# Performance work log

Hardware: AMD Instinct MI355X
Metric: run time of the kernel (lower is better)

The kernel has to match this reference:

```python
import jax, jax.numpy as jnp
import numpy as np

N_HEADS = 16
N_KV_HEADS = 4
HEAD_DIM = 128
ROPE_BASE = 10000.0


def _rms_norm(x):
    eps = jnp.asarray(jnp.finfo(x.dtype).eps, x.dtype)
    return x * jax.lax.rsqrt(jnp.mean(x * x, axis=-1, keepdims=True) + eps)


def _rope_tables(T, dtype):
    d = HEAD_DIM
    inv_freq = 1.0 / (ROPE_BASE ** (jnp.arange(0, d, 2, dtype=jnp.float32) / d))
    freqs = jnp.outer(jnp.arange(T, dtype=jnp.float32), inv_freq)  # [T, d/2]
    return jnp.cos(freqs).astype(dtype), jnp.sin(freqs).astype(dtype)


def _apply_rope(x, cos, sin):
    # x: [B, H, T, D]; cos/sin: [T, D/2]
    d = x.shape[-1] // 2
    x1, x2 = x[..., :d], x[..., d:]
    return jnp.concatenate((x1 * cos + x2 * sin, -x1 * sin + x2 * cos), axis=-1)


def setup_inputs() -> dict:
    key = jax.random.key(0)
    ks = jax.random.split(key, 5)
    B, T, C = 2, 2048, 2048
    kv_dim = N_KV_HEADS * HEAD_DIM
    s = 0.02
    return {
        "x": jax.random.normal(ks[0], (B, T, C), jnp.float32),
        "Wq": jax.random.normal(ks[1], (C, C), jnp.float32) * s,
        "Wk": jax.random.normal(ks[2], (kv_dim, C), jnp.float32) * s,
        "Wv": jax.random.normal(ks[3], (kv_dim, C), jnp.float32) * s,
        "Wo": jax.random.normal(ks[4], (C, C), jnp.float32) * s,
    }


def reference(x, Wq, Wk, Wv, Wo):
    B, T, C = x.shape
    g = N_HEADS // N_KV_HEADS

    # QKV projections (torch Linear: x @ W.T), split into heads -> [B, H, T, D]
    q = (x @ Wq.T).reshape(B, T, N_HEADS, HEAD_DIM).transpose(0, 2, 1, 3)
    k = (x @ Wk.T).reshape(B, T, N_KV_HEADS, HEAD_DIM).transpose(0, 2, 1, 3)
    v = (x @ Wv.T).reshape(B, T, N_KV_HEADS, HEAD_DIM).transpose(0, 2, 1, 3)

    # QK RMSNorm (no learned weight)
    q, k = _rms_norm(q), _rms_norm(k)

    # RoPE
    cos, sin = _rope_tables(T, q.dtype)
    q, k = _apply_rope(q, cos, sin), _apply_rope(k, cos, sin)

    # GQA: expand kv heads
    k = jnp.repeat(k, g, axis=1)
    v = jnp.repeat(v, g, axis=1)

    # causal SDPA
    scale = 1.0 / jnp.sqrt(jnp.asarray(HEAD_DIM, q.dtype))
    scores = jnp.einsum("bhqd,bhkd->bhqk", q, k) * scale
    mask = jnp.tril(jnp.ones((T, T), bool))
    scores = jnp.where(mask, scores, jnp.asarray(-jnp.inf, scores.dtype))
    att = jax.nn.softmax(scores, axis=-1)
    y = jnp.einsum("bhqk,bhkd->bhqd", att, v)

    y = y.transpose(0, 2, 1, 3).reshape(B, T, C)
    return y @ Wo.T
```

## Files before the change

### kernel.cpp

```cpp
#include <hip/hip_runtime.h>
#include <hip/hip_bf16.h>
#include <cstdint>
#include <math.h>

#define DEVINL __device__ __forceinline__

typedef __attribute__((ext_vector_type(8))) __bf16 bf16x8;
typedef __attribute__((ext_vector_type(4))) float floatx4;

constexpr int TB = 2;
constexpr int TT = 2048;
constexpr int TC = 2048;
constexpr int NH = 16, NKV = 4, HD = 128;
constexpr int MR = TB * TT;
constexpr int NQ = NH * HD;
constexpr int NK = NKV * HD;
constexpr int NQKV = NQ + 2 * NK;

DEVINL unsigned bfbits(float f) {
  unsigned u = __builtin_bit_cast(unsigned, f);
  return (u + 0x7FFFu + ((u >> 16) & 1u)) >> 16;
}
DEVINL int pk2(float a, float b) {
  union { __hip_bfloat162 h; int i; } u;
  u.h = __float22bfloat162_rn(float2{a, b});
  return u.i;
}
DEVINL void gl_lds16(const __hip_bfloat16* g, __hip_bfloat16* l) {
  __builtin_amdgcn_global_load_lds(
      (const __attribute__((address_space(1))) unsigned int*)g,
      (__attribute__((address_space(3))) unsigned int*)l, 16, 0, 0);
}
DEVINL floatx4 mfma16(bf16x8 a, bf16x8 b, floatx4 c) {
  return __builtin_amdgcn_mfma_f32_16x16x32_bf16(a, b, c, 0, 0, 0);
}
DEVINL void cstore(float* p, float v) { *p = v; }
DEVINL void cstore(__hip_bfloat16* p, float v) { *(unsigned short*)p = (unsigned short)bfbits(v); }

__global__ __launch_bounds__(256) void k_cvt5(
    const float* __restrict__ s0, const float* __restrict__ s1,
    const float* __restrict__ s2, const float* __restrict__ s3,
    const float* __restrict__ s4,
    __hip_bfloat16* __restrict__ d0, __hip_bfloat16* __restrict__ d1,
    __hip_bfloat16* __restrict__ d2, __hip_bfloat16* __restrict__ d3,
    __hip_bfloat16* __restrict__ d4) {
  const float* s;
  __hip_bfloat16* d;
  int n;
  switch (blockIdx.y) {
    case 0: s = s0; d = d0; n = MR * TC; break;
    case 1: s = s1; d = d1; n = NQ * TC; break;
    case 2: s = s2; d = d2; n = NK * TC; break;
    case 3: s = s3; d = d3; n = NK * TC; break;
    default: s = s4; d = d4; n = TC * TC; break;
  }
  int i = (blockIdx.x * 256 + threadIdx.x) * 4;
  if (i >= n) return;
  float4 v = *(const float4*)(s + i);
  ushort4 o;
  o.x = (unsigned short)bfbits(v.x);
  o.y = (unsigned short)bfbits(v.y);
  o.z = (unsigned short)bfbits(v.z);
  o.w = (unsigned short)bfbits(v.w);
  *(ushort4*)(d + i) = o;
}

template <typename OUT_T>
__global__ __launch_bounds__(256, 2) void k_gemm_bt(
    const __hip_bfloat16* __restrict__ A, const __hip_bfloat16* __restrict__ B,
    OUT_T* __restrict__ C, int M, int N, int K) {
  __shared__ __align__(16) __hip_bfloat16 As[128 * 32];
  __shared__ __align__(16) __hip_bfloat16 Bs[128 * 32];
  const int tid = threadIdx.x;
  const int lane = tid & 63, w = tid >> 6;
  const int q15 = lane & 15, quad = lane >> 4;
  const int wm = w >> 1, wn = w & 1;
  const int tm = blockIdx.y, tn = blockIdx.x;

  const int r0 = tid >> 2, c0 = (tid & 3) * 8;
  const __hip_bfloat16* a0 = A + (size_t)(tm * 128 + r0) * K + c0;
  const __hip_bfloat16* a1 = A + (size_t)(tm * 128 + r0 + 64) * K + c0;
  const __hip_bfloat16* b0 = B + (size_t)(tn * 128 + r0) * K + c0;
  const __hip_bfloat16* b1 = B + (size_t)(tn * 128 + r0 + 64) * K + c0;
  __hip_bfloat16* lA0 = As + (tid & ~63) * 8;
  __hip_bfloat16* lA1 = As + 2048 + (tid & ~63) * 8;
  __hip_bfloat16* lB0 = Bs + (tid & ~63) * 8;
  __hip_bfloat16* lB1 = Bs + 2048 + (tid & ~63) * 8;

  floatx4 acc[4][4] = {};
  for (int k0 = 0; k0 < K; k0 += 32) {
    __syncthreads();
    gl_lds16(a0 + k0, lA0);
    gl_lds16(a1 + k0, lA1);
    gl_lds16(b0 + k0, lB0);
    gl_lds16(b1 + k0, lB1);
    __syncthreads();
    bf16x8 af[4], bfr[4];
#pragma unroll
    for (int i = 0; i < 4; i++)
      af[i] = *(const bf16x8*)(As + (wm * 64 + i * 16 + q15) * 32 + quad * 8);
#pragma unroll
    for (int i = 0; i < 4; i++)
      bfr[i] = *(const bf16x8*)(Bs + (wn * 64 + i * 16 + q15) * 32 + quad * 8);
#pragma unroll
    for (int mi = 0; mi < 4; mi++)
#pragma unroll
      for (int ni = 0; ni < 4; ni++)
        acc[mi][ni] = mfma16(af[mi], bfr[ni], acc[mi][ni]);
  }
#pragma unroll
  for (int mi = 0; mi < 4; mi++) {
    int row0 = tm * 128 + wm * 64 + mi * 16 + quad * 4;
#pragma unroll
    for (int ni = 0; ni < 4; ni++) {
      int col = tn * 128 + wn * 64 + ni * 16 + q15;
#pragma unroll
      for (int r = 0; r < 4; r++)
        cstore(C + (size_t)(row0 + r) * N + col, acc[mi][ni][r]);
    }
  }
}

constexpr int ROPE_BLOCKS = (MR * 20) / 4;
__global__ __launch_bounds__(256) void k_prep(
    const __hip_bfloat16* __restrict__ qkv,
    __hip_bfloat16* __restrict__ q_l, __hip_bfloat16* __restrict__ k_l,
    __hip_bfloat16* __restrict__ vt) {
  if (blockIdx.x < ROPE_BLOCKS) {
    int gw = (blockIdx.x * 256 + threadIdx.x) >> 6;
    int lane = threadIdx.x & 63;
    int head = gw % 20;
    int bt = gw / 20;
    int b = bt >> 11, t = bt & (TT - 1);
    bool isq = head < NH;
    int h = isq ? head : head - NH;
    const __hip_bfloat16* src = qkv + (size_t)bt * NQKV + (isq ? h * HD : NQ + h * HD);
    float x1 = __bfloat162float(src[lane]);
    float x2 = __bfloat162float(src[lane + 64]);
    float ss = x1 * x1 + x2 * x2;
#pragma unroll
    for (int m = 1; m < 64; m <<= 1) ss += __shfl_xor(ss, m, 64);
    float rinv = rsqrtf(ss * (1.0f / 128.0f) + 1.1920928955078125e-07f);
    float ang = (float)t * exp2f((float)lane * -(13.287712379549449f / 64.0f));
    float sv = sinf(ang), cv = cosf(ang);
    float scale = isq ? (1.4426950408889634f * 0.08838834764831845f) : 1.0f;
    float o1 = (x1 * cv + x2 * sv) * rinv * scale;
    float o2 = (x2 * cv - x1 * sv) * rinv * scale;
    __hip_bfloat16* dst = isq ? q_l + ((size_t)(b * NH + h) * TT + t) * HD
                              : k_l + ((size_t)(b * NKV + h) * TT + t) * HD;
    *(unsigned short*)(dst + lane) = (unsigned short)bfbits(o1);
    *(unsigned short*)(dst + lane + 64) = (unsigned short)bfbits(o2);
  } else {
    __shared__ __hip_bfloat16 tile[64][130];
    int bid = blockIdx.x - ROPE_BLOCKS;
    int t0 = (bid & 31) * 64;
    int hk = (bid >> 5) & 3;
    int b = bid >> 7;
    int tid = threadIdx.x;
#pragma unroll
    for (int j = 0; j < 32; j++) {
      int e = j * 256 + tid;
      int tt = e >> 7, d = e & 127;
      tile[tt][d] = qkv[(size_t)(b * TT + t0 + tt) * NQKV + NQ + NK + hk * HD + d];
    }
    __syncthreads();
#pragma unroll
    for (int j = 0; j < 32; j++) {
      int e = j * 256 + tid;
      int d = e >> 6, tt = e & 63;
      vt[(((size_t)(b * NKV + hk)) * HD + d) * TT + t0 + tt] = tile[tt][d];
    }
  }
}

__global__ __launch_bounds__(256, 2) void k_attn(
    const __hip_bfloat16* __restrict__ q_l, const __hip_bfloat16* __restrict__ k_l,
    const __hip_bfloat16* __restrict__ vt_l, __hip_bfloat16* __restrict__ y) {
  __shared__ __align__(16) __hip_bfloat16 Ks[2][64 * 128];
  __shared__ __align__(16) __hip_bfloat16 Vs[2][128 * 64];
  __shared__ __align__(16) __hip_bfloat16 Ps[4][32 * 64];
  const int tid = threadIdx.x, lane = tid & 63, w = tid >> 6;
  const int q15 = lane & 15, quad = lane >> 4;
  const int id = blockIdx.x;
  const int qt = (TT / 128 - 1) - (id >> 5);
  const int h = id & 15, b = (id >> 4) & 1;
  const int hk = h >> 2;
  const int nkb = 2 * qt + 2;

  const __hip_bfloat16* kbase = k_l + (size_t)(b * NKV + hk) * TT * HD;
  const __hip_bfloat16* vbase = vt_l + (size_t)(b * NKV + hk) * HD * TT;
  const __hip_bfloat16* qbase = q_l + ((size_t)(b * NH + h) * TT + qt * 128) * HD;

  auto stage = [&](int kb, int buf) {
#pragma unroll
    for (int i = 0; i < 4; i++) {
      int s = i * 256 + tid;
      int rk = s >> 4, ck = s & 15;
      gl_lds16(kbase + (size_t)(kb * 64 + rk) * HD + (ck ^ (rk & 15)) * 8,
               Ks[buf] + (i * 256 + (tid & ~63)) * 8);
      int rv = s >> 3, cv = s & 7;
      gl_lds16(vbase + (size_t)rv * TT + kb * 64 + (cv ^ (rv & 7)) * 8,
               Vs[buf] + (i * 256 + (tid & ~63)) * 8);
    }
  };

  bf16x8 qf[4][2];
#pragma unroll
  for (int dc = 0; dc < 4; dc++)
#pragma unroll
    for (int qh = 0; qh < 2; qh++)
      qf[dc][qh] = *(const bf16x8*)(qbase + (size_t)(w * 32 + qh * 16 + q15) * HD +
                                    dc * 32 + quad * 8);

  __hip_bfloat16* pw = Ps[w];
  const int qrow0 = q15, qrow1 = 16 + q15;
  const int pw_c = 2 * 0 + (quad >> 1);
  const int pw_h = (quad & 1) * 4;

  floatx4 ot[8][2] = {};
  float lsum[2] = {0.0f, 0.0f};
  int cur = 0;
  const int kb_last_w = 2 * qt + (w >> 1);

  for (int kb = 0; kb < nkb; kb++) {
    __syncthreads();
    if (kb == 0) {
      stage(0, cur);
      __syncthreads();
    }
    if (kb + 1 < nkb) stage(kb + 1, cur ^ 1);

    if (kb <= kb_last_w) {
      floatx4 st[4][2] = {};
#pragma unroll
      for (int kt = 0; kt < 4; kt++) {
        int r = kt * 16 + q15;
#pragma unroll
        for (int dc = 0; dc < 4; dc++) {
          int c = dc * 4 + quad;
          bf16x8 kf = *(const bf16x8*)(Ks[cur] + (r * 16 + (c ^ (r & 15))) * 8);
          st[kt][0] = mfma16(kf, qf[dc][0], st[kt][0]);
          st[kt][1] = mfma16(kf, qf[dc][1], st[kt][1]);
        }
      }
      if (kb >= 2 * qt) {
#pragma unroll
        for (int qh = 0; qh < 2; qh++) {
          int qg = qt * 128 + w * 32 + qh * 16 + q15;
#pragma unroll
          for (int kt = 0; kt < 4; kt++)
#pragma unroll
            for (int r = 0; r < 4; r++)
              if (kb * 64 + kt * 16 + quad * 4 + r > qg) st[kt][qh][r] = -INFINITY;
        }
      }
#pragma unroll
      for (int kt = 0; kt < 4; kt++) {
#pragma unroll
        for (int qh = 0; qh < 2; qh++) {
          float p0 = exp2f(st[kt][qh][0]);
          float p1 = exp2f(st[kt][qh][1]);
          float p2 = exp2f(st[kt][qh][2]);
          float p3 = exp2f(st[kt][qh][3]);
          lsum[qh] += (p0 + p1) + (p2 + p3);
          int2 pv;
          pv.x = pk2(p0, p1);
          pv.y = pk2(p2, p3);
          int row = qh * 16 + q15;
          int c4 = (kt * 2 + (quad >> 1)) ^ (row & 7);
          *(int2*)(pw + row * 64 + c4 * 8 + pw_h) = pv;
        }
      }
#pragma unroll
      for (int kc = 0; kc < 2; kc++) {
        bf16x8 pf[2];
#pragma unroll
        for (int qh = 0; qh < 2; qh++) {
          int row = qh * 16 + q15;
          int c4 = (kc * 4 + quad) ^ (row & 7);
          pf[qh] = *(const bf16x8*)(pw + row * 64 + c4 * 8);
        }
#pragma unroll
        for (int dt = 0; dt < 8; dt++) {
          int r = dt * 16 + q15, c = kc * 4 + quad;
          bf16x8 vf = *(const bf16x8*)(Vs[cur] + (r * 8 + (c ^ (r & 7))) * 8);
          ot[dt][0] = mfma16(vf, pf[0], ot[dt][0]);
          ot[dt][1] = mfma16(vf, pf[1], ot[dt][1]);
        }
      }
    }
    cur ^= 1;
  }
#pragma unroll
  for (int qh = 0; qh < 2; qh++) {
    float ls = lsum[qh];
    ls += __shfl_xor(ls, 16, 64);
    ls += __shfl_xor(ls, 32, 64);
    float linv = 1.0f / ls;
    int t = qt * 128 + w * 32 + qh * 16 + q15;
    __hip_bfloat16* yrow = y + (size_t)(b * TT + t) * TC + h * HD;
#pragma unroll
    for (int dt = 0; dt < 8; dt++) {
      int d = dt * 16 + quad * 4;
      ushort4 o;
      o.x = (unsigned short)bfbits(ot[dt][qh][0] * linv);
      o.y = (unsigned short)bfbits(ot[dt][qh][1] * linv);
      o.z = (unsigned short)bfbits(ot[dt][qh][2] * linv);
      o.w = (unsigned short)bfbits(ot[dt][qh][3] * linv);
      *(ushort4*)(yrow + d) = o;
    }
  }
}

extern "C" void kernel_launch(void* const* d_in, const int* in_sizes, int n_in,
                              void* d_out, int out_size, void* d_ws, size_t ws_size,
                              hipStream_t stream) {
  (void)in_sizes; (void)n_in; (void)out_size; (void)ws_size;
  const float* x  = (const float*)d_in[0];
  const float* Wq = (const float*)d_in[1];
  const float* Wk = (const float*)d_in[2];
  const float* Wv = (const float*)d_in[3];
  const float* Wo = (const float*)d_in[4];
  float* out = (float*)d_out;

  char* ws = (char*)d_ws;
  size_t off = 0;
  auto alloc = [&](size_t bytes) {
    void* p = ws + off;
    off += (bytes + 255) & ~(size_t)255;
    return p;
  };
  __hip_bfloat16* xb   = (__hip_bfloat16*)alloc((size_t)MR * TC * 2);
  __hip_bfloat16* wqkv = (__hip_bfloat16*)alloc((size_t)NQKV * TC * 2);
  __hip_bfloat16* wo   = (__hip_bfloat16*)alloc((size_t)TC * TC * 2);
  __hip_bfloat16* qkv  = (__hip_bfloat16*)alloc((size_t)MR * NQKV * 2);
  __hip_bfloat16* q_l  = (__hip_bfloat16*)alloc((size_t)TB * NH * TT * HD * 2);
  __hip_bfloat16* k_l  = (__hip_bfloat16*)alloc((size_t)TB * NKV * TT * HD * 2);
  __hip_bfloat16* vt_l = (__hip_bfloat16*)alloc((size_t)TB * NKV * HD * TT * 2);
  __hip_bfloat16* yb   = (__hip_bfloat16*)alloc((size_t)MR * TC * 2);

  k_cvt5<<<dim3((MR * TC / 4 + 255) / 256, 5), 256, 0, stream>>>(
      x, Wq, Wk, Wv, Wo,
      xb, wqkv, wqkv + (size_t)NQ * TC, wqkv + (size_t)(NQ + NK) * TC, wo);

  k_gemm_bt<__hip_bfloat16><<<dim3(NQKV / 128, MR / 128), 256, 0, stream>>>(
      xb, wqkv, qkv, MR, NQKV, TC);

  k_prep<<<ROPE_BLOCKS + TB * NKV * (TT / 64), 256, 0, stream>>>(qkv, q_l, k_l, vt_l);

  k_attn<<<(TT / 128) * NH * TB, 256, 0, stream>>>(q_l, k_l, vt_l, yb);

  k_gemm_bt<float><<<dim3(TC / 128, MR / 128), 256, 0, stream>>>(
      yb, wo, out, MR, TC, TC);
}
```

Before: 319.3 us.

## Fuse QK RMSNorm, RoPE and V transpose into QKV GEMM epilogue

Replaces the QKV GEMM plus separate prep kernel with a dedicated GEMM whose warps each own 32 rows by a full 128-column head. This lets the epilogue compute the RMS norm, RoPE and scale in registers and write Q/K in head layout and V transposed directly. It removes the intermediate qkv buffer round trip and one kernel launch, at the cost of a different tile shape and sin/cos evaluation in the epilogue. It also changes the attention block ordering so the second half of the grid processes query tiles in ascending order.

```diff
diff --git a/kernel.cpp b/kernel.cpp
--- a/kernel.cpp
+++ b/kernel.cpp
@@ -121,54 +121,99 @@
   }
 }
 
-constexpr int ROPE_BLOCKS = (MR * 20) / 4;
-__global__ __launch_bounds__(256) void k_prep(
-    const __hip_bfloat16* __restrict__ qkv,
+__global__ __launch_bounds__(256, 2) void k_gemm_qkv(
+    const __hip_bfloat16* __restrict__ A, const __hip_bfloat16* __restrict__ B,
     __hip_bfloat16* __restrict__ q_l, __hip_bfloat16* __restrict__ k_l,
     __hip_bfloat16* __restrict__ vt) {
-  if (blockIdx.x < ROPE_BLOCKS) {
-    int gw = (blockIdx.x * 256 + threadIdx.x) >> 6;
-    int lane = threadIdx.x & 63;
-    int head = gw % 20;
-    int bt = gw / 20;
-    int b = bt >> 11, t = bt & (TT - 1);
-    bool isq = head < NH;
-    int h = isq ? head : head - NH;
-    const __hip_bfloat16* src = qkv + (size_t)bt * NQKV + (isq ? h * HD : NQ + h * HD);
-    float x1 = __bfloat162float(src[lane]);
-    float x2 = __bfloat162float(src[lane + 64]);
-    float ss = x1 * x1 + x2 * x2;
-#pragma unroll
-    for (int m = 1; m < 64; m <<= 1) ss += __shfl_xor(ss, m, 64);
-    float rinv = rsqrtf(ss * (1.0f / 128.0f) + 1.1920928955078125e-07f);
-    float ang = (float)t * exp2f((float)lane * -(13.287712379549449f / 64.0f));
-    float sv = sinf(ang), cv = cosf(ang);
-    float scale = isq ? (1.4426950408889634f * 0.08838834764831845f) : 1.0f;
-    float o1 = (x1 * cv + x2 * sv) * rinv * scale;
-    float o2 = (x2 * cv - x1 * sv) * rinv * scale;
-    __hip_bfloat16* dst = isq ? q_l + ((size_t)(b * NH + h) * TT + t) * HD
-                              : k_l + ((size_t)(b * NKV + h) * TT + t) * HD;
-    *(unsigned short*)(dst + lane) = (unsigned short)bfbits(o1);
-    *(unsigned short*)(dst + lane + 64) = (unsigned short)bfbits(o2);
+  __shared__ __align__(16) __hip_bfloat16 As[128 * 32];
+  __shared__ __align__(16) __hip_bfloat16 Bs[128 * 32];
+  const int K = TC;
+  const int tid = threadIdx.x;
+  const int lane = tid & 63, w = tid >> 6;
+  const int q15 = lane & 15, quad = lane >> 4;
+  const int tm = blockIdx.y, tn = blockIdx.x;
+  const int b = tm >> 4;
+
+  const int r0 = tid >> 2, c0 = (tid & 3) * 8;
+  const __hip_bfloat16* a0 = A + (size_t)(tm * 128 + r0) * K + c0;
+  const __hip_bfloat16* a1 = A + (size_t)(tm * 128 + r0 + 64) * K + c0;
+  const __hip_bfloat16* b0 = B + (size_t)(tn * 128 + r0) * K + c0;
+  const __hip_bfloat16* b1 = B + (size_t)(tn * 128 + r0 + 64) * K + c0;
+  __hip_bfloat16* lA0 = As + (tid & ~63) * 8;
+  __hip_bfloat16* lA1 = As + 2048 + (tid & ~63) * 8;
+  __hip_bfloat16* lB0 = Bs + (tid & ~63) * 8;
+  __hip_bfloat16* lB1 = Bs + 2048 + (tid & ~63) * 8;
+
+  floatx4 acc[2][8] = {};
+  for (int k0 = 0; k0 < K; k0 += 32) {
+    __syncthreads();
+    gl_lds16(a0 + k0, lA0);
+    gl_lds16(a1 + k0, lA1);
+    gl_lds16(b0 + k0, lB0);
+    gl_lds16(b1 + k0, lB1);
+    __syncthreads();
+    bf16x8 af[2], bfr[8];
+#pragma unroll
+    for (int i = 0; i < 2; i++)
+      af[i] = *(const bf16x8*)(As + (w * 32 + i * 16 + q15) * 32 + quad * 8);
+#pragma unroll
+    for (int i = 0; i < 8; i++)
+      bfr[i] = *(const bf16x8*)(Bs + (i * 16 + q15) * 32 + quad * 8);
+#pragma unroll
+    for (int mi = 0; mi < 2; mi++)
+#pragma unroll
+      for (int ni = 0; ni < 8; ni++)
+        acc[mi][ni] = mfma16(af[mi], bfr[ni], acc[mi][ni]);
+  }
+
+  const int trow0 = (tm & 15) * 128 + w * 32 + quad * 4;
+  if (tn < 20) {
+    const bool isq = tn < 16;
+    const float scale = isq ? (1.4426950408889634f * 0.08838834764831845f) : 1.0f;
+    __hip_bfloat16* dst = isq ? q_l + (size_t)(b * NH + tn) * TT * HD
+                              : k_l + (size_t)(b * NKV + (tn - 16)) * TT * HD;
+#pragma unroll
+    for (int mi = 0; mi < 2; mi++) {
+#pragma unroll
+      for (int r = 0; r < 4; r++) {
+        float ss = 0.f;
+#pragma unroll
+        for (int ni = 0; ni < 8; ni++) ss += acc[mi][ni][r] * acc[mi][ni][r];
+        ss += __shfl_xor(ss, 1, 64);
+        ss += __shfl_xor(ss, 2, 64);
+        ss += __shfl_xor(ss, 4, 64);
+        ss += __shfl_xor(ss, 8, 64);
+        float rinv = rsqrtf(ss * (1.0f / 128.0f) + 1.1920928955078125e-07f) * scale;
+        int t = trow0 + mi * 16 + r;
+        __hip_bfloat16* row = dst + (size_t)t * HD;
+#pragma unroll
+        for (int ni = 0; ni < 4; ni++) {
+          int d = ni * 16 + q15;
+          float ang = (float)t * exp2f((float)d * -(13.287712379549449f / 64.0f));
+          float sv = sinf(ang), cv = cosf(ang);
+          float x1 = acc[mi][ni][r], x2 = acc[mi][ni + 4][r];
+          float o1 = (x1 * cv + x2 * sv) * rinv;
+          float o2 = (x2 * cv - x1 * sv) * rinv;
+          *(unsigned short*)(row + d) = (unsigned short)bfbits(o1);
+          *(unsigned short*)(row + d + 64) = (unsigned short)bfbits(o2);
+        }
+      }
+    }
   } else {
-    __shared__ __hip_bfloat16 tile[64][130];
-    int bid = blockIdx.x - ROPE_BLOCKS;
-    int t0 = (bid & 31) * 64;
-    int hk = (bid >> 5) & 3;
-    int b = bid >> 7;
-    int tid = threadIdx.x;
-#pragma unroll
-    for (int j = 0; j < 32; j++) {
-      int e = j * 256 + tid;
-      int tt = e >> 7, d = e & 127;
-      tile[tt][d] = qkv[(size_t)(b * TT + t0 + tt) * NQKV + NQ + NK + hk * HD + d];
-    }
-    __syncthreads();
-#pragma unroll
-    for (int j = 0; j < 32; j++) {
-      int e = j * 256 + tid;
-      int d = e >> 6, tt = e & 63;
-      vt[(((size_t)(b * NKV + hk)) * HD + d) * TT + t0 + tt] = tile[tt][d];
+    __hip_bfloat16* vb = vt + (size_t)(b * NKV + (tn - 20)) * HD * TT;
+#pragma unroll
+    for (int mi = 0; mi < 2; mi++) {
+      int t0 = trow0 + mi * 16;
+#pragma unroll
+      for (int ni = 0; ni < 8; ni++) {
+        int d = ni * 16 + q15;
+        ushort4 o;
+        o.x = (unsigned short)bfbits(acc[mi][ni][0]);
+        o.y = (unsigned short)bfbits(acc[mi][ni][1]);
+        o.z = (unsigned short)bfbits(acc[mi][ni][2]);
+        o.w = (unsigned short)bfbits(acc[mi][ni][3]);
+        *(ushort4*)(vb + (size_t)d * TT + t0) = o;
+      }
     }
   }
 }
@@ -182,7 +227,7 @@
   const int tid = threadIdx.x, lane = tid & 63, w = tid >> 6;
   const int q15 = lane & 15, quad = lane >> 4;
   const int id = blockIdx.x;
-  const int qt = (TT / 128 - 1) - (id >> 5);
+  const int qt = (id < 256) ? (15 - (id >> 5)) : ((id - 256) >> 5);
   const int h = id & 15, b = (id >> 4) & 1;
   const int hk = h >> 2;
   const int nkb = 2 * qt + 2;
@@ -213,9 +258,6 @@
                                     dc * 32 + quad * 8);
 
   __hip_bfloat16* pw = Ps[w];
-  const int qrow0 = q15, qrow1 = 16 + q15;
-  const int pw_c = 2 * 0 + (quad >> 1);
-  const int pw_h = (quad & 1) * 4;
 
   floatx4 ot[8][2] = {};
   float lsum[2] = {0.0f, 0.0f};
@@ -268,7 +310,7 @@
           pv.y = pk2(p2, p3);
           int row = qh * 16 + q15;
           int c4 = (kt * 2 + (quad >> 1)) ^ (row & 7);
-          *(int2*)(pw + row * 64 + c4 * 8 + pw_h) = pv;
+          *(int2*)(pw + row * 64 + c4 * 8 + (quad & 1) * 4) = pv;
         }
       }
 #pragma unroll
@@ -333,7 +375,6 @@
   __hip_bfloat16* xb   = (__hip_bfloat16*)alloc((size_t)MR * TC * 2);
   __hip_bfloat16* wqkv = (__hip_bfloat16*)alloc((size_t)NQKV * TC * 2);
   __hip_bfloat16* wo   = (__hip_bfloat16*)alloc((size_t)TC * TC * 2);
-  __hip_bfloat16* qkv  = (__hip_bfloat16*)alloc((size_t)MR * NQKV * 2);
   __hip_bfloat16* q_l  = (__hip_bfloat16*)alloc((size_t)TB * NH * TT * HD * 2);
   __hip_bfloat16* k_l  = (__hip_bfloat16*)alloc((size_t)TB * NKV * TT * HD * 2);
   __hip_bfloat16* vt_l = (__hip_bfloat16*)alloc((size_t)TB * NKV * HD * TT * 2);
@@ -343,10 +384,8 @@
       x, Wq, Wk, Wv, Wo,
       xb, wqkv, wqkv + (size_t)NQ * TC, wqkv + (size_t)(NQ + NK) * TC, wo);
 
-  k_gemm_bt<__hip_bfloat16><<<dim3(NQKV / 128, MR / 128), 256, 0, stream>>>(
-      xb, wqkv, qkv, MR, NQKV, TC);
-
-  k_prep<<<ROPE_BLOCKS + TB * NKV * (TT / 64), 256, 0, stream>>>(qkv, q_l, k_l, vt_l);
+  k_gemm_qkv<<<dim3(NQKV / 128, MR / 128), 256, 0, stream>>>(
+      xb, wqkv, q_l, k_l, vt_l);
 
   k_attn<<<(TT / 128) * NH * TB, 256, 0, stream>>>(q_l, k_l, vt_l, yb);
 
```

After: 1.190 ms. 273% more time.
